# Kernel tuning notes

Measured on AMD Instinct MI355X. Metric: run time of the kernel, lower is better.

Reference implementation:

```python
import jax, jax.numpy as jnp
import numpy as np

N_COMP = 36          # sdf_n_comp
GRID = 300           # gridSize per axis
SDF_DIM = 256
APP_DIM = 128
MULTIRES = 3         # sdf positional-encoding octaves -> 3 + 3*2*3 = 21 channels
N_PTS = 524288       # sample points per batch (~1024 rays x 512 samples)
EMB_CH = 3 + 3 * 2 * MULTIRES            # 21
IN_CH = EMB_CH + 3 * N_COMP              # 129
OUT_CH = 1 + APP_DIM                     # 129 (sdf + appearance feature)
INIT_RADIUS = 0.2


def setup_inputs() -> dict:
    key = jax.random.key(0)
    ks = jax.random.split(key, 6)
    xyz_sampled = jax.random.uniform(ks[0], (N_PTS, 3), jnp.float32) * 2.0 - 1.0
    # tensor-decomposition grids (stacked over the 3 VM planes)
    planes = jax.random.normal(ks[1], (3, N_COMP, GRID, GRID), jnp.float32) * 0.1
    lines = jax.random.normal(ks[2], (3, N_COMP, GRID), jnp.float32) * (1.0 / (N_COMP * 3))
    # sdf_mat MLP params, initialized per init_mlp()
    w1 = jax.random.normal(ks[3], (SDF_DIM, IN_CH), jnp.float32) * (np.sqrt(2.0) / np.sqrt(SDF_DIM))
    b1 = jnp.zeros((SDF_DIM,), jnp.float32)
    w2 = jax.random.normal(ks[4], (OUT_CH, SDF_DIM), jnp.float32) * 1e-4 + np.sqrt(np.pi) / np.sqrt(SDF_DIM)
    b2 = jnp.full((OUT_CH,), -INIT_RADIUS, jnp.float32)
    return {"xyz_sampled": xyz_sampled, "planes": planes, "lines": lines,
            "w1": w1, "b1": b1, "w2": w2, "b2": b2}


def _bilin2d(plane, x, y):
    """Bilinear grid_sample, align_corners=True. plane [C,H,W]; x,y [N] in [-1,1] -> [C,N]."""
    C, H, W = plane.shape
    fx = (x + 1.0) * 0.5 * (W - 1)
    fy = (y + 1.0) * 0.5 * (H - 1)
    x0 = jnp.clip(jnp.floor(fx).astype(jnp.int32), 0, W - 2)
    y0 = jnp.clip(jnp.floor(fy).astype(jnp.int32), 0, H - 2)
    tx = fx - x0
    ty = fy - y0
    v00 = plane[:, y0, x0]
    v01 = plane[:, y0, x0 + 1]
    v10 = plane[:, y0 + 1, x0]
    v11 = plane[:, y0 + 1, x0 + 1]
    return (v00 * (1 - tx) * (1 - ty) + v01 * tx * (1 - ty)
            + v10 * (1 - tx) * ty + v11 * tx * ty)


def _lin1d(line, z):
    """Linear grid_sample, align_corners=True. line [C,L]; z [N] in [-1,1] -> [C,N]."""
    C, L = line.shape
    fz = (z + 1.0) * 0.5 * (L - 1)
    z0 = jnp.clip(jnp.floor(fz).astype(jnp.int32), 0, L - 2)
    tz = fz - z0
    return line[:, z0] * (1 - tz) + line[:, z0 + 1] * tz


def _embed(x):
    """NeRF positional encoding, include_input, octaves 2^0..2^(MULTIRES-1). [N,3] -> [N,21]."""
    freqs = 2.0 ** jnp.arange(MULTIRES, dtype=x.dtype)
    ang = x[:, :, None] * freqs  # [N,3,MULTIRES]
    n = x.shape[0]
    return jnp.concatenate([x, jnp.sin(ang).reshape(n, -1), jnp.cos(ang).reshape(n, -1)], axis=-1)


def reference(xyz_sampled, planes, lines, w1, b1, w2, b2):
    # aabb = [-1,1]^3 -> normalization is identity, kept explicit for faithfulness
    xn = (xyz_sampled - (-1.0)) / 2.0 * 2.0 - 1.0
    # matMode=[[0,1],[0,2],[1,2]], vecMode=[2,1,0]
    px = jnp.stack([xn[:, 0], xn[:, 0], xn[:, 1]])  # [3,N] first plane coord
    py = jnp.stack([xn[:, 1], xn[:, 2], xn[:, 2]])  # [3,N] second plane coord
    pz = jnp.stack([xn[:, 2], xn[:, 1], xn[:, 0]])  # [3,N] line coord
    pf = jax.vmap(_bilin2d)(planes, px, py)         # [3,C,N]
    lf = jax.vmap(_lin1d)(lines, pz)                # [3,C,N]
    feat = (pf * lf).transpose(2, 0, 1).reshape(xn.shape[0], -1)  # [N, 3*C]
    mlp_in = jnp.concatenate([_embed(xyz_sampled), feat], axis=-1)  # [N, 129]
    h = jax.nn.softplus(100.0 * (mlp_in @ w1.T + b1)) / 100.0       # Softplus(beta=100)
    out = h @ w2.T + b2                                             # [N, 1+app_dim]
    return out
```

## Files before the change

kernel.cpp:

```cpp
#include <hip/hip_runtime.h>
#include <cstdint>
#include <cstddef>


using half2v  = __attribute__((ext_vector_type(2))) _Float16;
using half4   = __attribute__((ext_vector_type(4))) _Float16;
using half8   = __attribute__((ext_vector_type(8))) _Float16;
using floatx4 = __attribute__((ext_vector_type(4))) float;

#define NPTS    524288
#define GRES    300
#define NCOMP   36
#define NCP     40
#define SDFD    256
#define IN_CH   129
#define OUT_CH  129
#define TILE_M  64
#define S_INL   168
#define S_OUT   136

#define OFF_W1S 0
#define SZ_W1S  (5*4*256*8*2)
#define OFF_W2S (OFF_W1S + SZ_W1S)
#define SZ_W2S  (8*4*144*8*2)
#define OFF_LT  (OFF_W2S + SZ_W2S)
#define SZ_LT   (3*GRES*NCP*2)
#define OFF_PLT (OFF_LT + SZ_LT)
#define SZ_PLT  ((size_t)3*GRES*GRES*NCP*2)
#define NEED_FAST ((size_t)OFF_PLT + SZ_PLT)


__global__ void prep_planes_k(const float* __restrict__ planes, _Float16* __restrict__ pl_t) {
    int idx = blockIdx.x * 256 + threadIdx.x;
    if (idx >= 3 * GRES * GRES) return;
    int x = idx % GRES; int t = idx / GRES; int y = t % GRES; int m = t / GRES;
    _Float16* dst = pl_t + (size_t)idx * NCP;
    const float* src = planes + (size_t)m * NCOMP * GRES * GRES + (size_t)y * GRES + x;
    #pragma unroll
    for (int j = 0; j < 5; ++j) {
        half8 o;
        #pragma unroll
        for (int e = 0; e < 8; ++e) {
            int c = j * 8 + e;
            o[e] = (c < NCOMP) ? (_Float16)src[(size_t)c * GRES * GRES] : (_Float16)0.f;
        }
        *(half8*)(dst + j * 8) = o;
    }
}

#define NB_W1 ((5*4*256*8 + 255)/256)
#define NB_W2 ((8*4*144*8 + 255)/256)
#define NB_L  ((3*GRES + 255)/256)
__global__ void prep_small_k(const float* __restrict__ w1, const float* __restrict__ w2,
                             const float* __restrict__ lines,
                             _Float16* __restrict__ w1s, _Float16* __restrict__ w2s,
                             _Float16* __restrict__ l_t) {
    int b = blockIdx.x;
    if (b < NB_W1) {
        int t = b * 256 + threadIdx.x;
        int j = t & 7; int n = (t >> 3) & 255; int q = t >> 11;
        int k = q * 8 + j;
        float v = 0.f;
        if (k < 120) {
            int m = k / 40, c = k % 40;
            if (c < NCOMP) v = w1[n * IN_CH + 21 + m * NCOMP + c];
        } else if (k < 141) {
            v = w1[n * IN_CH + (k - 120)];
        }
        w1s[t] = (_Float16)v;
    } else if (b < NB_W1 + NB_W2) {
        int t = (b - NB_W1) * 256 + threadIdx.x;
        if (t >= 8*4*144*8) return;
        int j = t & 7; int r = t >> 3; int n = r % 144; int q = r / 144;
        int k = q * 8 + j;
        float v = (n < OUT_CH) ? w2[n * SDFD + k] : 0.f;
        w2s[t] = (_Float16)v;
    } else {
        int idx = (b - NB_W1 - NB_W2) * 256 + threadIdx.x;
        if (idx >= 3 * GRES) return;
        int z = idx % GRES; int m = idx / GRES;
        _Float16* dst = l_t + (size_t)idx * NCP;
        const float* src = lines + ((size_t)m * NCOMP) * GRES + z;
        #pragma unroll
        for (int c = 0; c < NCOMP; ++c) dst[c] = (_Float16)src[(size_t)c * GRES];
        dst[36] = dst[37] = dst[38] = dst[39] = (_Float16)0.f;
    }
}


__device__ __forceinline__ float softplus100(float z) {
    return fmaxf(z, 0.f) + __logf(1.f + __expf(-fabsf(z)));
}

__device__ __forceinline__ void plane_coords(int m, float X, float Y, float Z,
                                             int& x0, int& y0, int& z0,
                                             float& tx, float& ty, float& tz) {
    const float px = (m == 2) ? Y : X;
    const float py = (m == 0) ? Y : Z;
    const float pz = (m == 0) ? Z : ((m == 1) ? Y : X);
    float fx = (px + 1.f) * 0.5f * 299.f;
    float fy = (py + 1.f) * 0.5f * 299.f;
    float fz = (pz + 1.f) * 0.5f * 299.f;
    x0 = (int)floorf(fx); x0 = x0 < 0 ? 0 : (x0 > 298 ? 298 : x0);
    y0 = (int)floorf(fy); y0 = y0 < 0 ? 0 : (y0 > 298 ? 298 : y0);
    z0 = (int)floorf(fz); z0 = z0 < 0 ? 0 : (z0 > 298 ? 298 : z0);
    tx = fx - (float)x0; ty = fy - (float)y0; tz = fz - (float)z0;
}

__device__ __forceinline__ void plane_gather_fast(
    int m, float X, float Y, float Z,
    const _Float16* __restrict__ pl_t, const _Float16* __restrict__ l_t,
    half8 f[5])
{
    int x0, y0, z0; float tx, ty, tz;
    plane_coords(m, X, Y, Z, x0, y0, z0, tx, ty, tz);
    const _Float16 h00 = (_Float16)((1.f - tx) * (1.f - ty));
    const _Float16 h01 = (_Float16)(tx * (1.f - ty));
    const _Float16 h10 = (_Float16)((1.f - tx) * ty);
    const _Float16 h11 = (_Float16)(tx * ty);
    const _Float16 hl0 = (_Float16)(1.f - tz), hl1 = (_Float16)tz;
    const half8 W00 = {h00,h00,h00,h00,h00,h00,h00,h00};
    const half8 W01 = {h01,h01,h01,h01,h01,h01,h01,h01};
    const half8 W10 = {h10,h10,h10,h10,h10,h10,h10,h10};
    const half8 W11 = {h11,h11,h11,h11,h11,h11,h11,h11};
    const half8 WL0 = {hl0,hl0,hl0,hl0,hl0,hl0,hl0,hl0};
    const half8 WL1 = {hl1,hl1,hl1,hl1,hl1,hl1,hl1,hl1};
    const _Float16* r0 = pl_t + ((size_t)(m * GRES + y0) * GRES + x0) * NCP;
    const _Float16* r1 = r0 + (size_t)GRES * NCP;
    const _Float16* lb = l_t + (size_t)(m * GRES + z0) * NCP;
    half8 a0[10], a1[10], al[10];
    #pragma unroll
    for (int j = 0; j < 10; ++j) a0[j] = *(const half8*)(r0 + 8 * j);
    #pragma unroll
    for (int j = 0; j < 10; ++j) a1[j] = *(const half8*)(r1 + 8 * j);
    half8 pf[5];
    #pragma unroll
    for (int j = 0; j < 5; ++j)
        pf[j] = a0[j] * W00 + a0[j + 5] * W01 + a1[j] * W10 + a1[j + 5] * W11;
    #pragma unroll
    for (int j = 0; j < 10; ++j) al[j] = *(const half8*)(lb + 8 * j);
    #pragma unroll
    for (int j = 0; j < 5; ++j) {
        half8 lf = al[j] * WL0 + al[j + 5] * WL1;
        f[j] = pf[j] * lf;
    }
}

__device__ __forceinline__ void plane_gather_slow(
    int m, float X, float Y, float Z,
    const float* __restrict__ planes, const float* __restrict__ lines,
    half8 f[5])
{
    int x0, y0, z0; float tx, ty, tz;
    plane_coords(m, X, Y, Z, x0, y0, z0, tx, ty, tz);
    const float w00 = (1.f - tx) * (1.f - ty), w01 = tx * (1.f - ty);
    const float w10 = (1.f - tx) * ty,         w11 = tx * ty;
    const float lw0 = 1.f - tz, lw1 = tz;
    #pragma unroll
    for (int j = 0; j < 5; ++j) f[j] = (half8){0,0,0,0,0,0,0,0};
    const float* pb = planes + (size_t)m * NCOMP * GRES * GRES;
    #pragma unroll
    for (int c = 0; c < NCOMP; ++c) {
        const float* pc = pb + (size_t)c * GRES * GRES + (size_t)y0 * GRES + x0;
        const float* lc = lines + ((size_t)m * NCOMP + c) * GRES + z0;
        float pf = pc[0] * w00 + pc[1] * w01 + pc[GRES] * w10 + pc[GRES + 1] * w11;
        float lf = lc[0] * lw0 + lc[1] * lw1;
        f[c >> 3][c & 7] = (_Float16)(pf * lf);
    }
}

__device__ __forceinline__ void embed_chunks(float X, float Y, float Z, half8 e[5]) {
    const float v3[3] = {X, Y, Z};
    _Float16 s[3][3], c[3][3];
    #pragma unroll
    for (int d = 0; d < 3; ++d) {
        float fm = 1.f;
        #pragma unroll
        for (int q = 0; q < 3; ++q) {
            const float a = v3[d] * fm;
            s[d][q] = (_Float16)__sinf(a);
            c[d][q] = (_Float16)__cosf(a);
            fm *= 2.f;
        }
    }
    const _Float16 z0 = (_Float16)0.f;
    e[0] = (half8){(_Float16)X, (_Float16)Y, (_Float16)Z, s[0][0], s[0][1], s[0][2], s[1][0], s[1][1]};
    e[1] = (half8){s[1][2], s[2][0], s[2][1], s[2][2], c[0][0], c[0][1], c[0][2], c[1][0]};
    e[2] = (half8){c[1][1], c[1][2], c[2][0], c[2][1], c[2][2], z0, z0, z0};
    e[3] = (half8){z0,z0,z0,z0,z0,z0,z0,z0};
    e[4] = (half8){z0,z0,z0,z0,z0,z0,z0,z0};
}


template <int FASTMODE>
__global__ __launch_bounds__(256, 3)
void tsdf_fused40_k(const float* __restrict__ xyz,
                    const float* __restrict__ planes, const float* __restrict__ lines,
                    const _Float16* __restrict__ pl_t, const _Float16* __restrict__ l_t,
                    const _Float16* __restrict__ w1s, const _Float16* __restrict__ w2s,
                    const float* __restrict__ b1, const float* __restrict__ b2,
                    float* __restrict__ out)
{
    __shared__ _Float16 lds_u[TILE_M * 272];
    _Float16* mlp_lds = lds_u;
    _Float16* h_lds   = lds_u;
    const int tid = threadIdx.x, blk = blockIdx.x;

    {
        const int p = tid >> 2, sub = tid & 3;
        const size_t gp = (size_t)blk * TILE_M + p;
        const float X = xyz[gp * 3 + 0];
        const float Y = xyz[gp * 3 + 1];
        const float Z = xyz[gp * 3 + 2];
        half8 f[5];
        int c0;
        if (sub < 3) {
            if (FASTMODE) plane_gather_fast(sub, X, Y, Z, pl_t, l_t, f);
            else          plane_gather_slow(sub, X, Y, Z, planes, lines, f);
            c0 = sub * 5;
        } else {
            embed_chunks(X, Y, Z, f);
            c0 = 15;
        }
        #pragma unroll
        for (int j = 0; j < 5; ++j)
            *(half8*)&mlp_lds[p * S_INL + (c0 + j) * 8] = f[j];
    }
    __syncthreads();

    const int lane = tid & 63, wv = tid >> 6, l15 = lane & 15, quad = lane >> 4;

    floatx4 acc1[4][4];
    #pragma unroll
    for (int mt = 0; mt < 4; ++mt)
        #pragma unroll
        for (int nt = 0; nt < 4; ++nt)
            acc1[mt][nt] = (floatx4){0.f, 0.f, 0.f, 0.f};

    #pragma unroll
    for (int s = 0; s < 5; ++s) {
        half8 a[4], b[4];
        #pragma unroll
        for (int mt = 0; mt < 4; ++mt)
            a[mt] = *(const half8*)&mlp_lds[(mt * 16 + l15) * S_INL + s * 32 + quad * 8];
        #pragma unroll
        for (int nt = 0; nt < 4; ++nt)
            b[nt] = *(const half8*)(w1s + ((size_t)((s * 4 + quad) * 256) + wv * 64 + nt * 16 + l15) * 8);
        #pragma unroll
        for (int mt = 0; mt < 4; ++mt)
            #pragma unroll
            for (int nt = 0; nt < 4; ++nt)
                acc1[mt][nt] = __builtin_amdgcn_mfma_f32_16x16x32_f16(a[mt], b[nt], acc1[mt][nt], 0, 0, 0);
    }
    __syncthreads();

    #pragma unroll
    for (int nt = 0; nt < 4; ++nt) {
        const int n = wv * 64 + nt * 16 + l15;
        const float bias = b1[n];
        #pragma unroll
        for (int mt = 0; mt < 4; ++mt) {
            #pragma unroll
            for (int r = 0; r < 4; ++r) {
                const int rowh = mt * 16 + quad * 4 + r;
                const float z = 100.f * (acc1[mt][nt][r] + bias);
                h_lds[(rowh * 256 + n) ^ ((rowh & 7) << 3)] = (_Float16)(softplus100(z) * 0.01f);
            }
        }
    }
    __syncthreads();

    floatx4 acc2[9];
    #pragma unroll
    for (int nt = 0; nt < 9; ++nt) acc2[nt] = (floatx4){0.f, 0.f, 0.f, 0.f};

    const int row2 = wv * 16 + l15;
    #pragma unroll
    for (int s = 0; s < 8; ++s) {
        const half8 a = *(const half8*)&h_lds[(row2 * 256 + s * 32 + quad * 8) ^ ((row2 & 7) << 3)];
        #pragma unroll
        for (int nt = 0; nt < 9; ++nt) {
            const half8 b = *(const half8*)(w2s + ((size_t)((s * 4 + quad) * 144) + nt * 16 + l15) * 8);
            acc2[nt] = __builtin_amdgcn_mfma_f32_16x16x32_f16(a, b, acc2[nt], 0, 0, 0);
        }
    }

    __syncthreads();
    float* o_lds = (float*)lds_u;
    const int m_lo = wv * 16 + quad * 4;
    #pragma unroll
    for (int nt = 0; nt < 9; ++nt) {
        const int n = nt * 16 + l15;
        if (n < OUT_CH) {
            const float bias = b2[n];
            #pragma unroll
            for (int r = 0; r < 4; ++r)
                o_lds[(m_lo + r) * S_OUT + n] = acc2[nt][r] + bias;
        }
    }
    __syncthreads();
    float* oblk = out + (size_t)blk * TILE_M * OUT_CH;
    #pragma unroll
    for (int c = 0; c < 33; ++c) {
        const int idx = c * 256 + tid;
        if (idx < TILE_M * OUT_CH) {
            const int row = idx / 129;
            const int col = idx - row * 129;
            __builtin_nontemporal_store(o_lds[row * S_OUT + col], &oblk[idx]);
        }
    }
}


extern "C" void kernel_launch(void* const* d_in, const int* in_sizes, int n_in,
                              void* d_out, int out_size, void* d_ws, size_t ws_size,
                              hipStream_t stream) {
    const float* xyz    = (const float*)d_in[0];
    const float* planes = (const float*)d_in[1];
    const float* lines  = (const float*)d_in[2];
    const float* w1     = (const float*)d_in[3];
    const float* b1     = (const float*)d_in[4];
    const float* w2     = (const float*)d_in[5];
    const float* b2     = (const float*)d_in[6];
    float* out = (float*)d_out;
    char* ws = (char*)d_ws;

    _Float16* w1s  = (_Float16*)(ws + OFF_W1S);
    _Float16* w2s  = (_Float16*)(ws + OFF_W2S);
    _Float16* l_t  = (_Float16*)(ws + OFF_LT);
    _Float16* pl_t = (_Float16*)(ws + OFF_PLT);

    const bool fast = (ws_size >= NEED_FAST);

    prep_small_k<<<NB_W1 + NB_W2 + NB_L, 256, 0, stream>>>(w1, w2, lines, w1s, w2s, l_t);

    if (fast) {
        prep_planes_k<<<(3 * GRES * GRES + 255) / 256, 256, 0, stream>>>(planes, pl_t);
        tsdf_fused40_k<1><<<NPTS / TILE_M, 256, 0, stream>>>(
            xyz, planes, lines, pl_t, l_t, w1s, w2s, b1, b2, out);
    } else {
        tsdf_fused40_k<0><<<NPTS / TILE_M, 256, 0, stream>>>(
            xyz, planes, lines, pl_t, l_t, w1s, w2s, b1, b2, out);
    }
}
```

Measured before the change: 551.5 us.

## Split plane gathers into per-chunk tasks and repartition second GEMM by N tiles

The gather phase now gives each thread one 8-channel chunk of one plane across four points, instead of one whole plane of one point. This spreads the wide scattered loads over more lanes and cuts per-thread register use. The xyz coordinates are loaded as vector floatx4 reads. The second MLP GEMM now splits its 9 output N-tiles across the four waves and each wave covers all 64 rows, so each B fragment from global memory is loaded once per block rather than once per wave. The cost is uneven work, since wave 0 gets 3 tiles and the others get 2.

```diff
diff --git a/kernel.cpp b/kernel.cpp
--- a/kernel.cpp
+++ b/kernel.cpp
@@ -107,68 +107,6 @@
     tx = fx - (float)x0; ty = fy - (float)y0; tz = fz - (float)z0;
 }
 
-__device__ __forceinline__ void plane_gather_fast(
-    int m, float X, float Y, float Z,
-    const _Float16* __restrict__ pl_t, const _Float16* __restrict__ l_t,
-    half8 f[5])
-{
-    int x0, y0, z0; float tx, ty, tz;
-    plane_coords(m, X, Y, Z, x0, y0, z0, tx, ty, tz);
-    const _Float16 h00 = (_Float16)((1.f - tx) * (1.f - ty));
-    const _Float16 h01 = (_Float16)(tx * (1.f - ty));
-    const _Float16 h10 = (_Float16)((1.f - tx) * ty);
-    const _Float16 h11 = (_Float16)(tx * ty);
-    const _Float16 hl0 = (_Float16)(1.f - tz), hl1 = (_Float16)tz;
-    const half8 W00 = {h00,h00,h00,h00,h00,h00,h00,h00};
-    const half8 W01 = {h01,h01,h01,h01,h01,h01,h01,h01};
-    const half8 W10 = {h10,h10,h10,h10,h10,h10,h10,h10};
-    const half8 W11 = {h11,h11,h11,h11,h11,h11,h11,h11};
-    const half8 WL0 = {hl0,hl0,hl0,hl0,hl0,hl0,hl0,hl0};
-    const half8 WL1 = {hl1,hl1,hl1,hl1,hl1,hl1,hl1,hl1};
-    const _Float16* r0 = pl_t + ((size_t)(m * GRES + y0) * GRES + x0) * NCP;
-    const _Float16* r1 = r0 + (size_t)GRES * NCP;
-    const _Float16* lb = l_t + (size_t)(m * GRES + z0) * NCP;
-    half8 a0[10], a1[10], al[10];
-    #pragma unroll
-    for (int j = 0; j < 10; ++j) a0[j] = *(const half8*)(r0 + 8 * j);
-    #pragma unroll
-    for (int j = 0; j < 10; ++j) a1[j] = *(const half8*)(r1 + 8 * j);
-    half8 pf[5];
-    #pragma unroll
-    for (int j = 0; j < 5; ++j)
-        pf[j] = a0[j] * W00 + a0[j + 5] * W01 + a1[j] * W10 + a1[j + 5] * W11;
-    #pragma unroll
-    for (int j = 0; j < 10; ++j) al[j] = *(const half8*)(lb + 8 * j);
-    #pragma unroll
-    for (int j = 0; j < 5; ++j) {
-        half8 lf = al[j] * WL0 + al[j + 5] * WL1;
-        f[j] = pf[j] * lf;
-    }
-}
-
-__device__ __forceinline__ void plane_gather_slow(
-    int m, float X, float Y, float Z,
-    const float* __restrict__ planes, const float* __restrict__ lines,
-    half8 f[5])
-{
-    int x0, y0, z0; float tx, ty, tz;
-    plane_coords(m, X, Y, Z, x0, y0, z0, tx, ty, tz);
-    const float w00 = (1.f - tx) * (1.f - ty), w01 = tx * (1.f - ty);
-    const float w10 = (1.f - tx) * ty,         w11 = tx * ty;
-    const float lw0 = 1.f - tz, lw1 = tz;
-    #pragma unroll
-    for (int j = 0; j < 5; ++j) f[j] = (half8){0,0,0,0,0,0,0,0};
-    const float* pb = planes + (size_t)m * NCOMP * GRES * GRES;
-    #pragma unroll
-    for (int c = 0; c < NCOMP; ++c) {
-        const float* pc = pb + (size_t)c * GRES * GRES + (size_t)y0 * GRES + x0;
-        const float* lc = lines + ((size_t)m * NCOMP + c) * GRES + z0;
-        float pf = pc[0] * w00 + pc[1] * w01 + pc[GRES] * w10 + pc[GRES + 1] * w11;
-        float lf = lc[0] * lw0 + lc[1] * lw1;
-        f[c >> 3][c & 7] = (_Float16)(pf * lf);
-    }
-}
-
 __device__ __forceinline__ void embed_chunks(float X, float Y, float Z, half8 e[5]) {
     const float v3[3] = {X, Y, Z};
     _Float16 s[3][3], c[3][3];
@@ -189,6 +127,10 @@
     e[2] = (half8){c[1][1], c[1][2], c[2][0], c[2][1], c[2][2], z0, z0, z0};
     e[3] = (half8){z0,z0,z0,z0,z0,z0,z0,z0};
     e[4] = (half8){z0,z0,z0,z0,z0,z0,z0,z0};
+}
+
+__device__ __forceinline__ half8 splat8(_Float16 v) {
+    return (half8){v, v, v, v, v, v, v, v};
 }
 
 
@@ -207,24 +149,69 @@
     const int tid = threadIdx.x, blk = blockIdx.x;
 
     {
-        const int p = tid >> 2, sub = tid & 3;
-        const size_t gp = (size_t)blk * TILE_M + p;
-        const float X = xyz[gp * 3 + 0];
-        const float Y = xyz[gp * 3 + 1];
-        const float Z = xyz[gp * 3 + 2];
-        half8 f[5];
-        int c0;
-        if (sub < 3) {
-            if (FASTMODE) plane_gather_fast(sub, X, Y, Z, pl_t, l_t, f);
-            else          plane_gather_slow(sub, X, Y, Z, planes, lines, f);
-            c0 = sub * 5;
-        } else {
-            embed_chunks(X, Y, Z, f);
-            c0 = 15;
-        }
-        #pragma unroll
-        for (int j = 0; j < 5; ++j)
-            *(half8*)&mlp_lds[p * S_INL + (c0 + j) * 8] = f[j];
+        const int task = tid & 15;
+        const int pb4  = (tid >> 4) * 4;
+        const int m    = task / 5;
+        const int j    = task - m * 5;
+        const float* xb = xyz + ((size_t)blk * TILE_M + pb4) * 3;
+        const floatx4 xv0 = *(const floatx4*)(xb);
+        const floatx4 xv1 = *(const floatx4*)(xb + 4);
+        const floatx4 xv2 = *(const floatx4*)(xb + 8);
+        #pragma unroll
+        for (int g = 0; g < 4; ++g) {
+            const int p = pb4 + g;
+            const float X = (g == 0) ? xv0[0] : (g == 1) ? xv0[3] : (g == 2) ? xv1[2] : xv2[1];
+            const float Y = (g == 0) ? xv0[1] : (g == 1) ? xv1[0] : (g == 2) ? xv1[3] : xv2[2];
+            const float Z = (g == 0) ? xv0[2] : (g == 1) ? xv1[1] : (g == 2) ? xv2[0] : xv2[3];
+            if (task < 15) {
+                int x0, y0, z0; float tx, ty, tz;
+                plane_coords(m, X, Y, Z, x0, y0, z0, tx, ty, tz);
+                if (FASTMODE) {
+                    const half8 W00 = splat8((_Float16)((1.f - tx) * (1.f - ty)));
+                    const half8 W01 = splat8((_Float16)(tx * (1.f - ty)));
+                    const half8 W10 = splat8((_Float16)((1.f - tx) * ty));
+                    const half8 W11 = splat8((_Float16)(tx * ty));
+                    const half8 WL0 = splat8((_Float16)(1.f - tz));
+                    const half8 WL1 = splat8((_Float16)tz);
+                    const _Float16* r0 = pl_t + ((size_t)(m * GRES + y0) * GRES + x0) * NCP + 8 * j;
+                    const _Float16* r1 = r0 + (size_t)GRES * NCP;
+                    const _Float16* lb = l_t + (size_t)(m * GRES + z0) * NCP + 8 * j;
+                    const half8 v00 = *(const half8*)(r0);
+                    const half8 v01 = *(const half8*)(r0 + NCP);
+                    const half8 v10 = *(const half8*)(r1);
+                    const half8 v11 = *(const half8*)(r1 + NCP);
+                    const half8 l0  = *(const half8*)(lb);
+                    const half8 l1  = *(const half8*)(lb + NCP);
+                    const half8 pf = v00 * W00 + v01 * W01 + v10 * W10 + v11 * W11;
+                    const half8 lf = l0 * WL0 + l1 * WL1;
+                    *(half8*)&mlp_lds[p * S_INL + task * 8] = pf * lf;
+                } else {
+                    const float w00 = (1.f - tx) * (1.f - ty), w01 = tx * (1.f - ty);
+                    const float w10 = (1.f - tx) * ty,         w11 = tx * ty;
+                    const float lw0 = 1.f - tz, lw1 = tz;
+                    half8 f;
+                    #pragma unroll
+                    for (int e = 0; e < 8; ++e) {
+                        const int c = j * 8 + e;
+                        float v = 0.f;
+                        if (c < NCOMP) {
+                            const float* pc = planes + ((size_t)(m * NCOMP + c) * GRES + y0) * GRES + x0;
+                            const float* lc = lines + ((size_t)m * NCOMP + c) * GRES + z0;
+                            const float pfv = pc[0] * w00 + pc[1] * w01 + pc[GRES] * w10 + pc[GRES + 1] * w11;
+                            v = pfv * (lc[0] * lw0 + lc[1] * lw1);
+                        }
+                        f[e] = (_Float16)v;
+                    }
+                    *(half8*)&mlp_lds[p * S_INL + task * 8] = f;
+                }
+            } else {
+                half8 e[5];
+                embed_chunks(X, Y, Z, e);
+                #pragma unroll
+                for (int jj = 0; jj < 5; ++jj)
+                    *(half8*)&mlp_lds[p * S_INL + (15 + jj) * 8] = e[jj];
+            }
+        }
     }
     __syncthreads();
 
@@ -270,32 +257,49 @@
     }
     __syncthreads();
 
-    floatx4 acc2[9];
-    #pragma unroll
-    for (int nt = 0; nt < 9; ++nt) acc2[nt] = (floatx4){0.f, 0.f, 0.f, 0.f};
-
-    const int row2 = wv * 16 + l15;
+    const int NTL = (wv == 0) ? 3 : 2;
+    floatx4 acc2[4][3];
+    #pragma unroll
+    for (int mt = 0; mt < 4; ++mt)
+        #pragma unroll
+        for (int ntl = 0; ntl < 3; ++ntl)
+            acc2[mt][ntl] = (floatx4){0.f, 0.f, 0.f, 0.f};
+
     #pragma unroll
     for (int s = 0; s < 8; ++s) {
-        const half8 a = *(const half8*)&h_lds[(row2 * 256 + s * 32 + quad * 8) ^ ((row2 & 7) << 3)];
-        #pragma unroll
-        for (int nt = 0; nt < 9; ++nt) {
-            const half8 b = *(const half8*)(w2s + ((size_t)((s * 4 + quad) * 144) + nt * 16 + l15) * 8);
-            acc2[nt] = __builtin_amdgcn_mfma_f32_16x16x32_f16(a, b, acc2[nt], 0, 0, 0);
+        half8 a[4];
+        #pragma unroll
+        for (int mt = 0; mt < 4; ++mt) {
+            const int rowh = mt * 16 + l15;
+            a[mt] = *(const half8*)&h_lds[(rowh * 256 + s * 32 + quad * 8) ^ ((rowh & 7) << 3)];
+        }
+        #pragma unroll
+        for (int ntl = 0; ntl < 3; ++ntl) {
+            if (ntl < NTL) {
+                const int ntg = wv + 4 * ntl;
+                const half8 b = *(const half8*)(w2s + ((size_t)((s * 4 + quad) * 144) + ntg * 16 + l15) * 8);
+                #pragma unroll
+                for (int mt = 0; mt < 4; ++mt)
+                    acc2[mt][ntl] = __builtin_amdgcn_mfma_f32_16x16x32_f16(a[mt], b, acc2[mt][ntl], 0, 0, 0);
+            }
         }
     }
 
     __syncthreads();
     float* o_lds = (float*)lds_u;
-    const int m_lo = wv * 16 + quad * 4;
-    #pragma unroll
-    for (int nt = 0; nt < 9; ++nt) {
-        const int n = nt * 16 + l15;
-        if (n < OUT_CH) {
-            const float bias = b2[n];
-            #pragma unroll
-            for (int r = 0; r < 4; ++r)
-                o_lds[(m_lo + r) * S_OUT + n] = acc2[nt][r] + bias;
+    #pragma unroll
+    for (int ntl = 0; ntl < 3; ++ntl) {
+        if (ntl < NTL) {
+            const int n = (wv + 4 * ntl) * 16 + l15;
+            if (n < OUT_CH) {
+                const float bias = b2[n];
+                #pragma unroll
+                for (int mt = 0; mt < 4; ++mt) {
+                    #pragma unroll
+                    for (int r = 0; r < 4; ++r)
+                        o_lds[(mt * 16 + quad * 4 + r) * S_OUT + n] = acc2[mt][ntl][r] + bias;
+                }
+            }
         }
     }
     __syncthreads();
```

Result: faster. 498.3 us (-9.7%).
